# Kernel tuning notes

Hardware: AMD Instinct MI355X
Metric: run time of the kernel (lower is better)

## Reference

```python
import jax, jax.numpy as jnp
import numpy as np

N, C, H, W = 32, 49, 9, 9   # batch, spectral bands (=outplane), spatial patch
MSIZE, K, PAD = 24, 7, 3    # conv3d out channels, spectral kernel, padding
EPS = 1e-5


def setup_inputs() -> dict:
    key = jax.random.key(0)
    k1, k2, k3 = jax.random.split(key, 3)
    x = jax.random.normal(k1, (N, C, H, W), dtype=jnp.float32)
    # Conv3d(1, MSIZE, [7,1,1]) params, PyTorch default uniform init
    fan_in = 1 * K * 1 * 1
    bound = 1.0 / np.sqrt(fan_in)
    conv_w = jax.random.uniform(k2, (MSIZE, 1, K, 1, 1), jnp.float32, -bound, bound)
    conv_b = jax.random.uniform(k3, (MSIZE,), jnp.float32, -bound, bound)
    # BatchNorm2d(49) affine params at init
    gamma = jnp.ones((C,), jnp.float32)
    beta = jnp.zeros((C,), jnp.float32)
    return {"x": x, "conv_w": conv_w, "conv_b": conv_b, "gamma": gamma, "beta": beta}


def reference(x, conv_w, conv_b, gamma, beta):
    n, c, h, w = x.shape
    # Conv3d over (depth=spectral, h, w) with kernel [K,1,1]: depth preserved
    x5 = x[:, None]  # (n,1,c,h,w)
    m = jax.lax.conv_general_dilated(
        x5, conv_w, window_strides=(1, 1, 1),
        padding=[(PAD, PAD), (0, 0), (0, 0)],
        dimension_numbers=("NCDHW", "OIDHW", "NCDHW"),
    ) + conv_b[None, :, None, None, None]        # (n, MSIZE, c, h, w)
    d = m.shape[1] * m.shape[2]                   # d = MSIZE * c
    mask = jax.nn.softmax(m.reshape(n, d, h * w), axis=-1).reshape(n, d, h, w)
    # original computes convm0 twice -> mask1 == mask0; reuse `mask` for both
    fk = jnp.einsum("ndhw,nchw->ncd", mask, x)    # (n, c, d)
    # out[n,c,h,w] = sum_d leaky_relu(fk[n,c,d] * mask[n,d,h,w])
    big = jnp.einsum("ncd,ndhw->ncdhw", fk, mask)  # (n,c,d,h,w) large intermediate
    out = jax.nn.leaky_relu(big, negative_slope=0.01).sum(axis=2)
    out = out + x                                  # residual
    # BatchNorm2d in training mode: batch statistics over (n,h,w) per channel
    mean = out.mean(axis=(0, 2, 3))
    var = out.var(axis=(0, 2, 3))
    out = (out - mean[:, None, None]) * jax.lax.rsqrt(var[:, None, None] + EPS)
    out = out * gamma[:, None, None] + beta[:, None, None]
    return out
```

## Files before the change

kernel.cpp:

```cpp
#include <hip/hip_runtime.h>
#include <hip/hip_bf16.h>

#define NN    32
#define CC    49
#define HWSZ  81
#define MSZ   24
#define KSZ   7
#define PADSZ 3
#define NHW   (NN*HWSZ)
#define NCHW  (NN*CC*HWSZ)

#define XSB_S  104
#define MSK_S  104
#define MSKT_S 72
#define G_S    72

typedef __attribute__((ext_vector_type(8))) short short8;
typedef __attribute__((ext_vector_type(4))) short short4v;
typedef __attribute__((ext_vector_type(4))) float f32x4;

__device__ __forceinline__ short f2b(float v) {
    unsigned u = __float_as_uint(v);
    u += 0x7fffu + ((u >> 16) & 1u);
    return (short)(u >> 16);
}

__global__ __launch_bounds__(256) void fuse_k1(
    const float* __restrict__ x, const float* __restrict__ cw,
    const float* __restrict__ cb, float* __restrict__ acc, int use_ws)
{
    __shared__ short xsb [64 * XSB_S];
    __shared__ short msk [64 * MSK_S];
    __shared__ short mskT[96 * MSKT_S];
    __shared__ short gm  [64 * G_S];

    const int o = blockIdx.x;
    const int n = blockIdx.y;
    const int t = threadIdx.x;
    const int lane = t & 63;
    const int wv = t >> 6;
    const int lr = lane & 15;
    const int lq = lane >> 4;

    {
        f32x4 z = {0.f, 0.f, 0.f, 0.f};
        for (int i = t; i < 832; i += 256) {
            ((f32x4*)xsb)[i] = z;
            ((f32x4*)msk)[i] = z;
        }
        for (int i = t; i < 864; i += 256)
            ((f32x4*)mskT)[i] = z;
    }

    const float* xg = x + (size_t)n * CC * HWSZ;
    float wk[KSZ];
    #pragma unroll
    for (int k = 0; k < KSZ; ++k) wk[k] = cw[o * KSZ + k];
    const float bias = cb[o];
    __syncthreads();

    for (int i = t; i < CC * HWSZ; i += 256) {
        int c = i / HWSZ, hw = i - c * HWSZ;
        xsb[c * XSB_S + hw] = f2b(xg[i]);
    }

    #pragma unroll
    for (int it = 0; it < 4; ++it) {
        int dd = it * 16 + wv * 4 + lq;
        if (dd < CC) {
            float a0 = 0.f, a1 = 0.f, a2 = 0.f, a3 = 0.f, a4 = 0.f, a5 = 0.f;
            #pragma unroll
            for (int k = 0; k < KSZ; ++k) {
                int r = dd + k - PADSZ;
                if (r >= 0 && r < CC) {
                    const float* xr = xg + r * HWSZ;
                    float w = wk[k];
                    a0 += w * xr[lr];
                    a1 += w * xr[lr + 16];
                    a2 += w * xr[lr + 32];
                    a3 += w * xr[lr + 48];
                    a4 += w * xr[lr + 64];
                    if (lr == 0) a5 += w * xr[80];
                }
            }
            a0 += bias; a1 += bias; a2 += bias; a3 += bias; a4 += bias;
            a5 = (lr == 0) ? (a5 + bias) : -1e30f;
            float mx = fmaxf(fmaxf(fmaxf(a0, a1), fmaxf(a2, a3)), fmaxf(a4, a5));
            #pragma unroll
            for (int off = 8; off; off >>= 1) mx = fmaxf(mx, __shfl_xor(mx, off, 64));
            float e0 = __expf(a0 - mx), e1 = __expf(a1 - mx), e2 = __expf(a2 - mx);
            float e3 = __expf(a3 - mx), e4 = __expf(a4 - mx);
            float e5 = (lr == 0) ? __expf(a5 - mx) : 0.f;
            float s = e0 + e1 + e2 + e3 + e4 + e5;
            #pragma unroll
            for (int off = 8; off; off >>= 1) s += __shfl_xor(s, off, 64);
            float inv = 1.f / s;
            short b0 = f2b(e0 * inv), b1 = f2b(e1 * inv), b2 = f2b(e2 * inv);
            short b3 = f2b(e3 * inv), b4 = f2b(e4 * inv);
            short* mrow = msk + dd * MSK_S;
            mrow[lr]      = b0;  mskT[(lr     ) * MSKT_S + dd] = b0;
            mrow[lr + 16] = b1;  mskT[(lr + 16) * MSKT_S + dd] = b1;
            mrow[lr + 32] = b2;  mskT[(lr + 32) * MSKT_S + dd] = b2;
            mrow[lr + 48] = b3;  mskT[(lr + 48) * MSKT_S + dd] = b3;
            mrow[lr + 64] = b4;  mskT[(lr + 64) * MSKT_S + dd] = b4;
            if (lr == 0) {
                short b5 = f2b(e5 * inv);
                mrow[80] = b5;   mskT[80 * MSKT_S + dd] = b5;
            }
        }
    }
    __syncthreads();

    {
        short8 a2[3];
        #pragma unroll
        for (int ks = 0; ks < 3; ++ks)
            a2[ks] = *(const short8*)&msk[(wv * 16 + lr) * MSK_S + ks * 32 + lq * 8];
        #pragma unroll
        for (int nt = 0; nt < 4; ++nt) {
            f32x4 accv = {0.f, 0.f, 0.f, 0.f};
            #pragma unroll
            for (int ks = 0; ks < 3; ++ks) {
                short8 b = *(const short8*)&xsb[(nt * 16 + lr) * XSB_S + ks * 32 + lq * 8];
                accv = __builtin_amdgcn_mfma_f32_16x16x32_bf16(a2[ks], b, accv, 0, 0, 0);
            }
            short4v pk;
            #pragma unroll
            for (int r = 0; r < 4; ++r) {
                float v = accv[r];
                v = (v >= 0.f) ? v : 0.01f * v;
                pk[r] = f2b(v);
            }
            *(short4v*)&gm[(nt * 16 + lr) * G_S + wv * 16 + lq * 4] = pk;
        }
    }
    __syncthreads();

    {
        float* dstn = use_ws ? (acc + (size_t)(o * NN + n) * CC * HWSZ)
                             : (acc + (size_t)n * CC * HWSZ);
        short8 a1[2];
        #pragma unroll
        for (int ks = 0; ks < 2; ++ks)
            a1[ks] = *(const short8*)&gm[(wv * 16 + lr) * G_S + ks * 32 + lq * 8];
        #pragma unroll
        for (int nt = 0; nt < 6; ++nt) {
            f32x4 accv = {0.f, 0.f, 0.f, 0.f};
            #pragma unroll
            for (int ks = 0; ks < 2; ++ks) {
                short8 b = *(const short8*)&mskT[(nt * 16 + lr) * MSKT_S + ks * 32 + lq * 8];
                accv = __builtin_amdgcn_mfma_f32_16x16x32_bf16(a1[ks], b, accv, 0, 0, 0);
            }
            int hw = nt * 16 + lr;
            if (hw < HWSZ) {
                int cb = wv * 16 + lq * 4;
                if (use_ws) {
                    #pragma unroll
                    for (int r = 0; r < 4; ++r) {
                        int c = cb + r;
                        if (c < CC) dstn[c * HWSZ + hw] = accv[r];
                    }
                } else {
                    #pragma unroll
                    for (int r = 0; r < 4; ++r) {
                        int c = cb + r;
                        if (c < CC) atomicAdd(dstn + c * HWSZ + hw, accv[r]);
                    }
                }
            }
        }
    }
}

__global__ __launch_bounds__(1024) void fuse_k2w(
    const float* __restrict__ ws, const float* __restrict__ x,
    const float* __restrict__ gamma, const float* __restrict__ beta,
    float* __restrict__ out)
{
    const int c = blockIdx.x;
    const int t = threadIdx.x;
    float vals[3];
    float sum = 0.f, sq = 0.f;
    int cnt = 0;
    for (int i = t; i < NHW; i += 1024) {
        int n = i / HWSZ;
        int hw = i - n * HWSZ;
        int idx = (n * CC + c) * HWSZ + hw;
        const float* p = ws + idx;
        float v = x[idx];
        #pragma unroll
        for (int o = 0; o < MSZ; ++o) v += p[(size_t)o * NCHW];
        vals[cnt++] = v;
        sum += v; sq += v * v;
    }
    #pragma unroll
    for (int off = 32; off; off >>= 1) {
        sum += __shfl_xor(sum, off, 64);
        sq  += __shfl_xor(sq, off, 64);
    }
    __shared__ float rs[16], rq[16];
    const int lane = t & 63, wv = t >> 6;
    if (lane == 0) { rs[wv] = sum; rq[wv] = sq; }
    __syncthreads();
    float ts = 0.f, tq = 0.f;
    #pragma unroll
    for (int w = 0; w < 16; ++w) { ts += rs[w]; tq += rq[w]; }
    const float invD = 1.f / (float)NHW;
    float mean = ts * invD;
    float var  = tq * invD - mean * mean;
    float scal = rsqrtf(var + 1e-5f) * gamma[c];
    float shft = beta[c] - mean * scal;
    cnt = 0;
    for (int i = t; i < NHW; i += 1024) {
        int n = i / HWSZ;
        int hw = i - n * HWSZ;
        out[(n * CC + c) * HWSZ + hw] = vals[cnt++] * scal + shft;
    }
}

__global__ __launch_bounds__(1024) void fuse_k2(
    float* __restrict__ out, const float* __restrict__ x,
    const float* __restrict__ gamma, const float* __restrict__ beta)
{
    const int c = blockIdx.x;
    const int t = threadIdx.x;
    float vals[3];
    float sum = 0.f, sq = 0.f;
    int cnt = 0;
    for (int i = t; i < NHW; i += 1024) {
        int n = i / HWSZ;
        int hw = i - n * HWSZ;
        int idx = (n * CC + c) * HWSZ + hw;
        float v = out[idx] + x[idx];
        vals[cnt++] = v;
        sum += v; sq += v * v;
    }
    #pragma unroll
    for (int off = 32; off; off >>= 1) {
        sum += __shfl_xor(sum, off, 64);
        sq  += __shfl_xor(sq, off, 64);
    }
    __shared__ float rs[16], rq[16];
    const int lane = t & 63, wv = t >> 6;
    if (lane == 0) { rs[wv] = sum; rq[wv] = sq; }
    __syncthreads();
    float ts = 0.f, tq = 0.f;
    #pragma unroll
    for (int w = 0; w < 16; ++w) { ts += rs[w]; tq += rq[w]; }
    const float invD = 1.f / (float)NHW;
    float mean = ts * invD;
    float var  = tq * invD - mean * mean;
    float scal = rsqrtf(var + 1e-5f) * gamma[c];
    float shft = beta[c] - mean * scal;
    cnt = 0;
    for (int i = t; i < NHW; i += 1024) {
        int n = i / HWSZ;
        int hw = i - n * HWSZ;
        out[(n * CC + c) * HWSZ + hw] = vals[cnt++] * scal + shft;
    }
}

extern "C" void kernel_launch(void* const* d_in, const int* in_sizes, int n_in,
                              void* d_out, int out_size, void* d_ws, size_t ws_size,
                              hipStream_t stream) {
    const float* x     = (const float*)d_in[0];
    const float* cw    = (const float*)d_in[1];
    const float* cb    = (const float*)d_in[2];
    const float* gamma = (const float*)d_in[3];
    const float* beta  = (const float*)d_in[4];
    float* out = (float*)d_out;

    const size_t need = (size_t)MSZ * NCHW * sizeof(float);
    if (ws_size >= need) {
        float* ws = (float*)d_ws;
        fuse_k1<<<dim3(MSZ, NN), 256, 0, stream>>>(x, cw, cb, ws, 1);
        fuse_k2w<<<CC, 1024, 0, stream>>>(ws, x, gamma, beta, out);
    } else {
        hipMemsetAsync(out, 0, (size_t)NCHW * sizeof(float), stream);
        fuse_k1<<<dim3(MSZ, NN), 256, 0, stream>>>(x, cw, cb, out, 0);
        fuse_k2<<<CC, 1024, 0, stream>>>(out, x, gamma, beta);
    }
}
```

Before: 85.04 us.

## Split reduce/BatchNorm into multi-block stats pass and elementwise normalize; conv from LDS

The single per-channel BatchNorm kernel (49 blocks of 1024 threads) is replaced by two kernels. The first runs 49x4 blocks that sum the 24 partial workspace slices plus the residual, write the pre-norm output, and atomically accumulate per-channel sum and sum-of-squares. The second applies the normalization elementwise over a flat grid. Separately, the spectral conv in fuse_k1 now reads the bf16 copy of x from shared memory instead of global fp32, after an added barrier. This aims to raise parallelism in the bandwidth-bound reduction at the cost of an extra launch and an extra pass over the output. It also lowers conv input precision to bf16 and relies on stats being zeroed by one block of fuse_k1 before any fuse_k2a atomics.

```diff
diff --git a/kernel.cpp b/kernel.cpp
--- a/kernel.cpp
+++ b/kernel.cpp
@@ -24,10 +24,14 @@
     u += 0x7fffu + ((u >> 16) & 1u);
     return (short)(u >> 16);
 }
+__device__ __forceinline__ float b2f(short s) {
+    return __uint_as_float(((unsigned)(unsigned short)s) << 16);
+}
 
 __global__ __launch_bounds__(256) void fuse_k1(
     const float* __restrict__ x, const float* __restrict__ cw,
-    const float* __restrict__ cb, float* __restrict__ acc, int use_ws)
+    const float* __restrict__ cb, float* __restrict__ acc,
+    float* __restrict__ stats, int use_ws)
 {
     __shared__ short xsb [64 * XSB_S];
     __shared__ short msk [64 * MSK_S];
@@ -42,6 +46,8 @@
     const int lr = lane & 15;
     const int lq = lane >> 4;
 
+    if (use_ws && o == 0 && n == 0 && t < 98) stats[t] = 0.f;
+
     {
         f32x4 z = {0.f, 0.f, 0.f, 0.f};
         for (int i = t; i < 832; i += 256) {
@@ -63,6 +69,7 @@
         int c = i / HWSZ, hw = i - c * HWSZ;
         xsb[c * XSB_S + hw] = f2b(xg[i]);
     }
+    __syncthreads();
 
     #pragma unroll
     for (int it = 0; it < 4; ++it) {
@@ -73,14 +80,14 @@
             for (int k = 0; k < KSZ; ++k) {
                 int r = dd + k - PADSZ;
                 if (r >= 0 && r < CC) {
-                    const float* xr = xg + r * HWSZ;
+                    const short* xr = xsb + r * XSB_S;
                     float w = wk[k];
-                    a0 += w * xr[lr];
-                    a1 += w * xr[lr + 16];
-                    a2 += w * xr[lr + 32];
-                    a3 += w * xr[lr + 48];
-                    a4 += w * xr[lr + 64];
-                    if (lr == 0) a5 += w * xr[80];
+                    a0 += w * b2f(xr[lr]);
+                    a1 += w * b2f(xr[lr + 16]);
+                    a2 += w * b2f(xr[lr + 32]);
+                    a3 += w * b2f(xr[lr + 48]);
+                    a4 += w * b2f(xr[lr + 64]);
+                    if (lr == 0) a5 += w * b2f(xr[80]);
                 }
             }
             a0 += bias; a1 += bias; a2 += bias; a3 += bias; a4 += bias;
@@ -172,25 +179,22 @@
     }
 }
 
-__global__ __launch_bounds__(1024) void fuse_k2w(
+__global__ __launch_bounds__(256) void fuse_k2a(
     const float* __restrict__ ws, const float* __restrict__ x,
-    const float* __restrict__ gamma, const float* __restrict__ beta,
-    float* __restrict__ out)
+    float* __restrict__ out, float* __restrict__ stats)
 {
     const int c = blockIdx.x;
+    const int s = blockIdx.y;
     const int t = threadIdx.x;
-    float vals[3];
     float sum = 0.f, sq = 0.f;
-    int cnt = 0;
-    for (int i = t; i < NHW; i += 1024) {
-        int n = i / HWSZ;
-        int hw = i - n * HWSZ;
+    for (int i = t; i < 8 * HWSZ; i += 256) {
+        int n = 8 * s + i / HWSZ;
+        int hw = i - (i / HWSZ) * HWSZ;
         int idx = (n * CC + c) * HWSZ + hw;
-        const float* p = ws + idx;
         float v = x[idx];
         #pragma unroll
-        for (int o = 0; o < MSZ; ++o) v += p[(size_t)o * NCHW];
-        vals[cnt++] = v;
+        for (int o = 0; o < MSZ; ++o) v += ws[(size_t)o * NCHW + idx];
+        out[idx] = v;
         sum += v; sq += v * v;
     }
     #pragma unroll
@@ -198,23 +202,30 @@
         sum += __shfl_xor(sum, off, 64);
         sq  += __shfl_xor(sq, off, 64);
     }
-    __shared__ float rs[16], rq[16];
+    __shared__ float rs[4], rq[4];
     const int lane = t & 63, wv = t >> 6;
     if (lane == 0) { rs[wv] = sum; rq[wv] = sq; }
     __syncthreads();
-    float ts = 0.f, tq = 0.f;
-    #pragma unroll
-    for (int w = 0; w < 16; ++w) { ts += rs[w]; tq += rq[w]; }
-    const float invD = 1.f / (float)NHW;
-    float mean = ts * invD;
-    float var  = tq * invD - mean * mean;
-    float scal = rsqrtf(var + 1e-5f) * gamma[c];
-    float shft = beta[c] - mean * scal;
-    cnt = 0;
-    for (int i = t; i < NHW; i += 1024) {
-        int n = i / HWSZ;
-        int hw = i - n * HWSZ;
-        out[(n * CC + c) * HWSZ + hw] = vals[cnt++] * scal + shft;
+    if (t == 0) {
+        float ts = rs[0] + rs[1] + rs[2] + rs[3];
+        float tq = rq[0] + rq[1] + rq[2] + rq[3];
+        atomicAdd(&stats[c], ts);
+        atomicAdd(&stats[CC + c], tq);
+    }
+}
+
+__global__ __launch_bounds__(256) void fuse_k2b(
+    float* __restrict__ out, const float* __restrict__ stats,
+    const float* __restrict__ gamma, const float* __restrict__ beta)
+{
+    int i = blockIdx.x * 256 + threadIdx.x;
+    if (i < NCHW) {
+        int c = (i / HWSZ) % CC;
+        const float invD = 1.f / (float)NHW;
+        float mean = stats[c] * invD;
+        float var  = stats[CC + c] * invD - mean * mean;
+        float scal = rsqrtf(var + 1e-5f) * gamma[c];
+        out[i] = (out[i] - mean) * scal + beta[c];
     }
 }
 
@@ -270,14 +281,16 @@
     const float* beta  = (const float*)d_in[4];
     float* out = (float*)d_out;
 
-    const size_t need = (size_t)MSZ * NCHW * sizeof(float);
+    const size_t need = (size_t)MSZ * NCHW * sizeof(float) + 2 * CC * sizeof(float);
     if (ws_size >= need) {
-        float* ws = (float*)d_ws;
-        fuse_k1<<<dim3(MSZ, NN), 256, 0, stream>>>(x, cw, cb, ws, 1);
-        fuse_k2w<<<CC, 1024, 0, stream>>>(ws, x, gamma, beta, out);
+        float* ws    = (float*)d_ws;
+        float* stats = ws + (size_t)MSZ * NCHW;
+        fuse_k1<<<dim3(MSZ, NN), 256, 0, stream>>>(x, cw, cb, ws, stats, 1);
+        fuse_k2a<<<dim3(CC, 4), 256, 0, stream>>>(ws, x, out, stats);
+        fuse_k2b<<<(NCHW + 255) / 256, 256, 0, stream>>>(out, stats, gamma, beta);
     } else {
         hipMemsetAsync(out, 0, (size_t)NCHW * sizeof(float), stream);
-        fuse_k1<<<dim3(MSZ, NN), 256, 0, stream>>>(x, cw, cb, out, 0);
+        fuse_k1<<<dim3(MSZ, NN), 256, 0, stream>>>(x, cw, cb, out, nullptr, 0);
         fuse_k2<<<CC, 1024, 0, stream>>>(out, x, gamma, beta);
     }
 }
```

Result: no change. 85.51 us (+0.6%).

## Transpose workspace to channel-innermost, compute conv from LDS, trim LDS zeroing

Applied to the files above, without the earlier changes.

The workspace is reordered so the MSZ conv-channel partials for each (n,c,hw) sit contiguously. The reduction kernel can then read them as six float4 loads instead of 24 strided loads. The spectral conv now reads the bf16 copy of x already staged in shared memory rather than global memory, using vectorized short4 loads. Only the padding regions of the x tile are zeroed, and that zeroing is merged with the staging before a single barrier. The cost is that the first kernel's workspace stores now have a 96-byte stride across lanes, which makes them less coalesced. The conv input also loses precision because it is now bf16 rather than fp32.

```diff
diff --git a/kernel.cpp b/kernel.cpp
--- a/kernel.cpp
+++ b/kernel.cpp
@@ -24,6 +24,9 @@
     u += 0x7fffu + ((u >> 16) & 1u);
     return (short)(u >> 16);
 }
+__device__ __forceinline__ float b2f(short s) {
+    return __uint_as_float(((unsigned)(unsigned short)s) << 16);
+}
 
 __global__ __launch_bounds__(256) void fuse_k1(
     const float* __restrict__ x, const float* __restrict__ cw,
@@ -42,27 +45,31 @@
     const int lr = lane & 15;
     const int lq = lane >> 4;
 
-    {
-        f32x4 z = {0.f, 0.f, 0.f, 0.f};
-        for (int i = t; i < 832; i += 256) {
-            ((f32x4*)xsb)[i] = z;
-            ((f32x4*)msk)[i] = z;
-        }
-        for (int i = t; i < 864; i += 256)
-            ((f32x4*)mskT)[i] = z;
-    }
-
     const float* xg = x + (size_t)n * CC * HWSZ;
     float wk[KSZ];
     #pragma unroll
     for (int k = 0; k < KSZ; ++k) wk[k] = cw[o * KSZ + k];
     const float bias = cb[o];
-    __syncthreads();
-
+
+    const f32x4 z4 = {0.f, 0.f, 0.f, 0.f};
     for (int i = t; i < CC * HWSZ; i += 256) {
         int c = i / HWSZ, hw = i - c * HWSZ;
         xsb[c * XSB_S + hw] = f2b(xg[i]);
     }
+    if (t < CC) {
+        short* row = xsb + t * XSB_S;
+        #pragma unroll
+        for (int cq = 81; cq < 88; ++cq) row[cq] = 0;
+        *(f32x4*)(row + 88) = z4;
+        *(f32x4*)(row + 96) = z4;
+    }
+    for (int j = t; j < 15 * 13; j += 256) {
+        int rr = j / 13, cg = j - rr * 13;
+        *(f32x4*)(xsb + (49 + rr) * XSB_S + cg * 8) = z4;
+    }
+    for (int i = t; i < 832; i += 256) ((f32x4*)msk)[i] = z4;
+    for (int i = t; i < 864; i += 256) ((f32x4*)mskT)[i] = z4;
+    __syncthreads();
 
     #pragma unroll
     for (int it = 0; it < 4; ++it) {
@@ -73,14 +80,15 @@
             for (int k = 0; k < KSZ; ++k) {
                 int r = dd + k - PADSZ;
                 if (r >= 0 && r < CC) {
-                    const float* xr = xg + r * HWSZ;
+                    const short* xr = xsb + r * XSB_S;
+                    short4v xa = *(const short4v*)(xr + 4 * lr);
                     float w = wk[k];
-                    a0 += w * xr[lr];
-                    a1 += w * xr[lr + 16];
-                    a2 += w * xr[lr + 32];
-                    a3 += w * xr[lr + 48];
-                    a4 += w * xr[lr + 64];
-                    if (lr == 0) a5 += w * xr[80];
+                    a0 += w * b2f(xa[0]);
+                    a1 += w * b2f(xa[1]);
+                    a2 += w * b2f(xa[2]);
+                    a3 += w * b2f(xa[3]);
+                    a4 += w * b2f(xr[64 + lr]);
+                    if (lr == 0) a5 += w * b2f(xr[80]);
                 }
             }
             a0 += bias; a1 += bias; a2 += bias; a3 += bias; a4 += bias;
@@ -95,17 +103,22 @@
             #pragma unroll
             for (int off = 8; off; off >>= 1) s += __shfl_xor(s, off, 64);
             float inv = 1.f / s;
-            short b0 = f2b(e0 * inv), b1 = f2b(e1 * inv), b2 = f2b(e2 * inv);
-            short b3 = f2b(e3 * inv), b4 = f2b(e4 * inv);
+            short4v pk;
+            pk[0] = f2b(e0 * inv); pk[1] = f2b(e1 * inv);
+            pk[2] = f2b(e2 * inv); pk[3] = f2b(e3 * inv);
+            short b4 = f2b(e4 * inv);
             short* mrow = msk + dd * MSK_S;
-            mrow[lr]      = b0;  mskT[(lr     ) * MSKT_S + dd] = b0;
-            mrow[lr + 16] = b1;  mskT[(lr + 16) * MSKT_S + dd] = b1;
-            mrow[lr + 32] = b2;  mskT[(lr + 32) * MSKT_S + dd] = b2;
-            mrow[lr + 48] = b3;  mskT[(lr + 48) * MSKT_S + dd] = b3;
-            mrow[lr + 64] = b4;  mskT[(lr + 64) * MSKT_S + dd] = b4;
+            *(short4v*)(mrow + 4 * lr) = pk;
+            mrow[64 + lr] = b4;
+            mskT[(4 * lr    ) * MSKT_S + dd] = pk[0];
+            mskT[(4 * lr + 1) * MSKT_S + dd] = pk[1];
+            mskT[(4 * lr + 2) * MSKT_S + dd] = pk[2];
+            mskT[(4 * lr + 3) * MSKT_S + dd] = pk[3];
+            mskT[(64 + lr   ) * MSKT_S + dd] = b4;
             if (lr == 0) {
                 short b5 = f2b(e5 * inv);
-                mrow[80] = b5;   mskT[80 * MSKT_S + dd] = b5;
+                mrow[80] = b5;
+                mskT[80 * MSKT_S + dd] = b5;
             }
         }
     }
@@ -137,7 +150,7 @@
     __syncthreads();
 
     {
-        float* dstn = use_ws ? (acc + (size_t)(o * NN + n) * CC * HWSZ)
+        float* accn = use_ws ? (acc + (size_t)n * CC * HWSZ * MSZ)
                              : (acc + (size_t)n * CC * HWSZ);
         short8 a1[2];
         #pragma unroll
@@ -158,13 +171,14 @@
                     #pragma unroll
                     for (int r = 0; r < 4; ++r) {
                         int c = cb + r;
-                        if (c < CC) dstn[c * HWSZ + hw] = accv[r];
+                        if (c < CC)
+                            accn[(size_t)(c * HWSZ + hw) * MSZ + o] = accv[r];
                     }
                 } else {
                     #pragma unroll
                     for (int r = 0; r < 4; ++r) {
                         int c = cb + r;
-                        if (c < CC) atomicAdd(dstn + c * HWSZ + hw, accv[r]);
+                        if (c < CC) atomicAdd(accn + c * HWSZ + hw, accv[r]);
                     }
                 }
             }
@@ -186,10 +200,12 @@
         int n = i / HWSZ;
         int hw = i - n * HWSZ;
         int idx = (n * CC + c) * HWSZ + hw;
-        const float* p = ws + idx;
-        float v = x[idx];
-        #pragma unroll
-        for (int o = 0; o < MSZ; ++o) v += p[(size_t)o * NCHW];
+        const float4* p = (const float4*)(ws + (size_t)idx * MSZ);
+        float4 s0 = p[0], s1 = p[1], s2 = p[2], s3 = p[3], s4 = p[4], s5 = p[5];
+        float v = x[idx]
+                + (s0.x + s0.y + s0.z + s0.w) + (s1.x + s1.y + s1.z + s1.w)
+                + (s2.x + s2.y + s2.z + s2.w) + (s3.x + s3.y + s3.z + s3.w)
+                + (s4.x + s4.y + s4.z + s4.w) + (s5.x + s5.y + s5.z + s5.w);
         vals[cnt++] = v;
         sum += v; sq += v * v;
     }
```

After: 99.12 us. +16.6%, slower.
